# Optimization experiments

Measured on AMD Instinct MI355X. Metric: run time of the kernel, lower is better.

## Reference

```python
import jax, jax.numpy as jnp
import numpy as np

N, T, C, K = 32, 1024, 512, 64
EPS = 1e-12  # torch F.normalize eps


def _l2norm(v, axis):
    n = jnp.sqrt(jnp.sum(v * v, axis=axis, keepdims=True))
    return v / jnp.maximum(n, EPS)


def setup_inputs() -> dict:
    key = jax.random.key(0)
    k1, k2 = jax.random.split(key)
    x = jax.random.normal(k1, (N, T, C), dtype=jnp.float32)
    centroids = jax.random.uniform(k2, (K, C), dtype=jnp.float32)
    # mirrors _init_params: conv.weight = 0.2*centroids, conv.bias = -0.1*||centroids||
    W = 0.2 * centroids
    b = -0.1 * jnp.sqrt(jnp.sum(centroids * centroids, axis=1))
    return {"x": x, "W": W, "b": b, "centroids": centroids}


def reference(x, W, b, centroids):
    # x: [N, T, C] -> [N, C, T]
    xt = jnp.transpose(x, (0, 2, 1))
    # 1x1 Conv1d == per-timestep linear: logits [N, K, T]
    logits = jnp.einsum('kc,nct->nkt', W, xt) + b[None, :, None]
    a = jax.nn.softmax(logits, axis=1)  # softmax over clusters
    # vlad[n,k,c] = sum_t a[n,k,t] * (x[n,c,t] - centroid[k,c])
    #            = (a @ x^T) - sum_t(a) * centroid  (GEMM form, same math)
    vlad = jnp.einsum('nkt,nct->nkc', a, xt) - a.sum(axis=-1)[:, :, None] * centroids[None]
    vlad = _l2norm(vlad, axis=2)          # intra-normalization per cluster
    vlad = vlad.reshape(vlad.shape[0], -1)
    vlad = _l2norm(vlad, axis=1)          # global L2 normalization
    return vlad
```

## Files before the change

kernel.cpp:

```cpp
#include <hip/hip_runtime.h>
#include <cmath>

namespace {

constexpr int N = 32, T = 1024, C = 512, K = 64;
constexpr float EPS = 1e-12f;

typedef short s8v __attribute__((ext_vector_type(8)));
typedef short s4v __attribute__((ext_vector_type(4)));
typedef short s2v __attribute__((ext_vector_type(2)));
typedef float f4v __attribute__((ext_vector_type(4)));

__device__ inline unsigned short f2bh(float f) {
  __bf16 h = (__bf16)f;
  return __builtin_bit_cast(unsigned short, h);
}
__device__ inline float bh2f(unsigned short u) {
  __bf16 h = __builtin_bit_cast(__bf16, u);
  return (float)h;
}

#define MFMA16(A, B, Cc) __builtin_amdgcn_mfma_f32_16x16x32_bf16((A), (B), (Cc), 0, 0, 0)

__global__ __launch_bounds__(256, 4) void k_gemm1(
    const float* __restrict__ x, const float* __restrict__ W,
    const float* __restrict__ b, unsigned short* __restrict__ aTh,
    unsigned short* __restrict__ aTl, float* __restrict__ asum_part) {
  __shared__ __align__(16) unsigned short sm0[4 * 64 * 72];
  __shared__ __align__(16) unsigned short sm1[4 * 64 * 72];
  __shared__ float asum_l[256];

  const int tid = threadIdx.x;
  const int w = tid >> 6, lane = tid & 63, lm = lane & 15, lq = lane >> 4;
  const int th = w >> 1;
  const int kh = w & 1;
  const long r0 = (long)blockIdx.x * 64;
  const int n = blockIdx.x >> 4, tl = blockIdx.x & 15;

  f4v acc[2][2] = {};
  float4 px0[4], pw0[4], px1[4], pw1[4];

#define G1_LOAD(s, c0)                                                       \
  {                                                                          \
    _Pragma("unroll") for (int r = 0; r < 4; ++r) {                          \
      const int f = tid + r * 256, t = f >> 4, cg = f & 15;                  \
      px##s[r] = *(const float4*)&x[(r0 + t) * C + (c0) + cg * 4];           \
      pw##s[r] = *(const float4*)&W[(long)t * C + (c0) + cg * 4];            \
    }                                                                        \
  }

#define G1_STAGE(buf, s)                                                     \
  {                                                                          \
    unsigned short* xh_s = (buf);                                            \
    unsigned short* xl_s = (buf) + 64 * 72;                                  \
    unsigned short* wh_s = (buf) + 2 * 64 * 72;                              \
    unsigned short* wl_s = (buf) + 3 * 64 * 72;                              \
    _Pragma("unroll") for (int r = 0; r < 4; ++r) {                          \
      const int f = tid + r * 256, t = f >> 4, cg = f & 15;                  \
      const float ex[4] = {px##s[r].x, px##s[r].y, px##s[r].z, px##s[r].w};  \
      const float ew[4] = {pw##s[r].x, pw##s[r].y, pw##s[r].z, pw##s[r].w};  \
      s4v xh, xl, wh, wl;                                                    \
      _Pragma("unroll") for (int i = 0; i < 4; ++i) {                        \
        unsigned short hb = f2bh(ex[i]);                                     \
        xh[i] = (short)hb; xl[i] = (short)f2bh(ex[i] - bh2f(hb));            \
        hb = f2bh(ew[i]);                                                    \
        wh[i] = (short)hb; wl[i] = (short)f2bh(ew[i] - bh2f(hb));            \
      }                                                                      \
      *(s4v*)&xh_s[t * 72 + cg * 4] = xh;                                    \
      *(s4v*)&xl_s[t * 72 + cg * 4] = xl;                                    \
      *(s4v*)&wh_s[t * 72 + cg * 4] = wh;                                    \
      *(s4v*)&wl_s[t * 72 + cg * 4] = wl;                                    \
    }                                                                        \
  }

#define G1_MFMA(buf)                                                         \
  {                                                                          \
    unsigned short* xh_s = (buf);                                            \
    unsigned short* xl_s = (buf) + 64 * 72;                                  \
    unsigned short* wh_s = (buf) + 2 * 64 * 72;                              \
    unsigned short* wl_s = (buf) + 3 * 64 * 72;                              \
    _Pragma("unroll") for (int ks = 0; ks < 2; ++ks) {                       \
      const int col = ks * 32 + lq * 8;                                      \
      s8v ah[2], al[2], bh[2], bl[2];                                        \
      _Pragma("unroll") for (int i = 0; i < 2; ++i) {                        \
        ah[i] = *(const s8v*)&xh_s[(th * 32 + i * 16 + lm) * 72 + col];      \
        al[i] = *(const s8v*)&xl_s[(th * 32 + i * 16 + lm) * 72 + col];      \
        bh[i] = *(const s8v*)&wh_s[(kh * 32 + i * 16 + lm) * 72 + col];      \
        bl[i] = *(const s8v*)&wl_s[(kh * 32 + i * 16 + lm) * 72 + col];      \
      }                                                                      \
      _Pragma("unroll") for (int i = 0; i < 2; ++i)                          \
          _Pragma("unroll") for (int j = 0; j < 2; ++j) {                    \
        acc[i][j] = MFMA16(ah[i], bh[j], acc[i][j]);                         \
        acc[i][j] = MFMA16(ah[i], bl[j], acc[i][j]);                         \
        acc[i][j] = MFMA16(al[i], bh[j], acc[i][j]);                         \
      }                                                                      \
    }                                                                        \
  }

  G1_LOAD(0, 0);
  G1_STAGE(sm0, 0);
  G1_LOAD(1, 64);
  __syncthreads();
  for (int c0 = 0; c0 < C; c0 += 128) {
    if (c0 + 128 < C) G1_LOAD(0, c0 + 128);
    G1_STAGE(sm1, 1);
    G1_MFMA(sm0);
    __syncthreads();
    if (c0 + 192 < C) G1_LOAD(1, c0 + 192);
    if (c0 + 128 < C) G1_STAGE(sm0, 0);
    G1_MFMA(sm1);
    __syncthreads();
  }
#undef G1_LOAD
#undef G1_STAGE
#undef G1_MFMA

  float* Ls = (float*)sm0;
  unsigned short* L2h = sm1;
  unsigned short* L2l = sm1 + 64 * 72;
  const float bias[2] = {b[kh * 32 + lm], b[kh * 32 + 16 + lm]};
#pragma unroll
  for (int i = 0; i < 2; ++i)
#pragma unroll
    for (int j = 0; j < 2; ++j)
#pragma unroll
      for (int r = 0; r < 4; ++r)
        Ls[(th * 32 + i * 16 + lq * 4 + r) * 68 + kh * 32 + j * 16 + lm] =
            acc[i][j][r] + bias[j];
  __syncthreads();

  {
    const int row = tid >> 2, q = tid & 3;
    float av[16];
#pragma unroll
    for (int u = 0; u < 4; ++u)
      *(float4*)&av[u * 4] = *(const float4*)&Ls[row * 68 + q * 16 + u * 4];
    float m = av[0];
#pragma unroll
    for (int i = 1; i < 16; ++i) m = fmaxf(m, av[i]);
    m = fmaxf(m, __shfl_xor(m, 1, 64));
    m = fmaxf(m, __shfl_xor(m, 2, 64));
    float sum = 0.f;
#pragma unroll
    for (int i = 0; i < 16; ++i) {
      av[i] = __expf(av[i] - m);
      sum += av[i];
    }
    sum += __shfl_xor(sum, 1, 64);
    sum += __shfl_xor(sum, 2, 64);
    const float inv = 1.f / sum;
    float ps[16];
#pragma unroll
    for (int i = 0; i < 16; ++i) {
      av[i] *= inv;
      ps[i] = av[i];
      const unsigned short hb = f2bh(av[i]);
      L2h[(q * 16 + i) * 72 + row] = hb;
      L2l[(q * 16 + i) * 72 + row] = f2bh(av[i] - bh2f(hb));
    }
#pragma unroll
    for (int s = 4; s < 64; s <<= 1)
#pragma unroll
      for (int i = 0; i < 16; ++i) ps[i] += __shfl_xor(ps[i], s, 64);
    if (lane < 4) {
#pragma unroll
      for (int i = 0; i < 16; ++i) asum_l[w * 64 + q * 16 + i] = ps[i];
    }
  }
  __syncthreads();

  if (tid < 64) {
    asum_part[(n * 16 + tl) * 64 + tid] = asum_l[tid] + asum_l[64 + tid] +
                                          asum_l[128 + tid] + asum_l[192 + tid];
  }
  {
    const int k = tid >> 2, tg = tid & 3;
    const long gb = ((long)n * K + k) * T + tl * 64 + tg * 16;
    *(s8v*)&aTh[gb] = *(const s8v*)&L2h[k * 72 + tg * 16];
    *(s8v*)&aTh[gb + 8] = *(const s8v*)&L2h[k * 72 + tg * 16 + 8];
    *(s8v*)&aTl[gb] = *(const s8v*)&L2l[k * 72 + tg * 16];
    *(s8v*)&aTl[gb + 8] = *(const s8v*)&L2l[k * 72 + tg * 16 + 8];
  }
}

__global__ __launch_bounds__(256, 4) void k_gemm2(
    const float* __restrict__ x, const unsigned short* __restrict__ aTh,
    const unsigned short* __restrict__ aTl,
    const float* __restrict__ asum_part, const float* __restrict__ cent,
    float* __restrict__ vlad, float* __restrict__ ssq_part) {
  __shared__ __align__(16) unsigned short smA[(2 * 64 + 2 * 32) * 72];
  __shared__ __align__(16) unsigned short smB[(2 * 64 + 2 * 32) * 72];
  __shared__ float asum_l[64];
  __shared__ float ssq_l[128];

  const int tid = threadIdx.x;
  const int w = tid >> 6, lane = tid & 63, lm = lane & 15, lq = lane >> 4;
  const int kh = w >> 1;
  const int ch = w & 1;
  const int p = blockIdx.x;
  const int g = p >> 3;
  const int n = ((g & 3) << 3) | (p & 7);
  const int cq = g >> 2;
  const int c0 = cq * 32;

  if (tid < 64) {
    float s = 0.f;
#pragma unroll
    for (int tl = 0; tl < 16; ++tl) s += asum_part[(n * 16 + tl) * 64 + tid];
    asum_l[tid] = s;
  }

  f4v acc[2] = {};
  const int ak = tid >> 2, atg = tid & 3;
  s8v pah0[2], pal0[2], pah1[2], pal1[2];
  float4 px0[2], px1[2];

#define G2_LOAD(s, t0)                                                       \
  {                                                                          \
    const long ab = ((long)n * K + ak) * T + (t0) + atg * 16;                \
    pah##s[0] = *(const s8v*)&aTh[ab];                                       \
    pah##s[1] = *(const s8v*)&aTh[ab + 8];                                   \
    pal##s[0] = *(const s8v*)&aTl[ab];                                       \
    pal##s[1] = *(const s8v*)&aTl[ab + 8];                                   \
    const int cg = tid & 7, tq = tid >> 3;                                   \
    _Pragma("unroll") for (int i = 0; i < 2; ++i)                            \
        px##s[i] = *(const float4*)&x[((long)n * T + (t0) + tq * 2 + i) * C +\
                                      c0 + cg * 4];                          \
  }

#define G2_STAGE(buf, s)                                                     \
  {                                                                          \
    unsigned short* ah_s = (buf);                                            \
    unsigned short* al_s = (buf) + 64 * 72;                                  \
    unsigned short* xh_s = (buf) + 2 * 64 * 72;                              \
    unsigned short* xl_s = (buf) + 2 * 64 * 72 + 32 * 72;                    \
    *(s8v*)&ah_s[ak * 72 + atg * 16] = pah##s[0];                            \
    *(s8v*)&ah_s[ak * 72 + atg * 16 + 8] = pah##s[1];                        \
    *(s8v*)&al_s[ak * 72 + atg * 16] = pal##s[0];                            \
    *(s8v*)&al_s[ak * 72 + atg * 16 + 8] = pal##s[1];                        \
    const int cg = tid & 7, tq = tid >> 3;                                   \
    _Pragma("unroll") for (int cc = 0; cc < 4; ++cc) {                       \
      s2v h, l;                                                              \
      _Pragma("unroll") for (int i = 0; i < 2; ++i) {                        \
        const float e = ((const float*)&px##s[i])[cc];                       \
        const unsigned short hb = f2bh(e);                                   \
        h[i] = (short)hb;                                                    \
        l[i] = (short)f2bh(e - bh2f(hb));                                    \
      }                                                                      \
      *(s2v*)&xh_s[(cg * 4 + cc) * 72 + tq * 2] = h;                         \
      *(s2v*)&xl_s[(cg * 4 + cc) * 72 + tq * 2] = l;                         \
    }                                                                        \
  }

#define G2_MFMA(buf)                                                         \
  {                                                                          \
    unsigned short* ah_s = (buf);                                            \
    unsigned short* al_s = (buf) + 64 * 72;                                  \
    unsigned short* xh_s = (buf) + 2 * 64 * 72;                              \
    unsigned short* xl_s = (buf) + 2 * 64 * 72 + 32 * 72;                    \
    _Pragma("unroll") for (int ks = 0; ks < 2; ++ks) {                       \
      const int col = ks * 32 + lq * 8;                                      \
      s8v ah[2], al[2];                                                      \
      _Pragma("unroll") for (int i = 0; i < 2; ++i) {                        \
        ah[i] = *(const s8v*)&ah_s[(kh * 32 + i * 16 + lm) * 72 + col];      \
        al[i] = *(const s8v*)&al_s[(kh * 32 + i * 16 + lm) * 72 + col];      \
      }                                                                      \
      const s8v bh = *(const s8v*)&xh_s[(ch * 16 + lm) * 72 + col];          \
      const s8v bl = *(const s8v*)&xl_s[(ch * 16 + lm) * 72 + col];          \
      _Pragma("unroll") for (int i = 0; i < 2; ++i) {                        \
        acc[i] = MFMA16(ah[i], bh, acc[i]);                                  \
        acc[i] = MFMA16(ah[i], bl, acc[i]);                                  \
        acc[i] = MFMA16(al[i], bh, acc[i]);                                  \
      }                                                                      \
    }                                                                        \
  }

  G2_LOAD(0, 0);
  G2_STAGE(smA, 0);
  G2_LOAD(1, 64);
  __syncthreads();
  for (int t0 = 0; t0 < T; t0 += 128) {
    if (t0 + 128 < T) G2_LOAD(0, t0 + 128);
    G2_STAGE(smB, 1);
    G2_MFMA(smA);
    __syncthreads();
    if (t0 + 192 < T) G2_LOAD(1, t0 + 192);
    if (t0 + 128 < T) G2_STAGE(smA, 0);
    G2_MFMA(smB);
    __syncthreads();
  }
#undef G2_LOAD
#undef G2_STAGE
#undef G2_MFMA

  float ssqp[2][4];
#pragma unroll
  for (int i = 0; i < 2; ++i) {
#pragma unroll
    for (int r = 0; r < 4; ++r) {
      const int k = kh * 32 + i * 16 + lq * 4 + r;
      const float as = asum_l[k];
      const int c = c0 + ch * 16 + lm;
      const float v = acc[i][r] - as * cent[(long)k * C + c];
      vlad[((long)n * K + k) * C + c] = v;
      ssqp[i][r] = v * v;
    }
  }
#pragma unroll
  for (int i = 0; i < 2; ++i)
#pragma unroll
    for (int r = 0; r < 4; ++r) {
      float s = ssqp[i][r];
      s += __shfl_xor(s, 1, 64);
      s += __shfl_xor(s, 2, 64);
      s += __shfl_xor(s, 4, 64);
      s += __shfl_xor(s, 8, 64);
      ssqp[i][r] = s;
    }
  if (lm == 0) {
#pragma unroll
    for (int i = 0; i < 2; ++i)
#pragma unroll
      for (int r = 0; r < 4; ++r)
        ssq_l[(kh * 32 + i * 16 + lq * 4 + r) * 2 + ch] = ssqp[i][r];
  }
  __syncthreads();
  if (tid < 64)
    ssq_part[(n * 16 + cq) * 64 + tid] = ssq_l[tid * 2] + ssq_l[tid * 2 + 1];
}

__global__ __launch_bounds__(256) void k_norm(
    const float* __restrict__ vlad, const float* __restrict__ ssq_part,
    float* __restrict__ out) {
  __shared__ float denom[64];
  __shared__ float contrib[64];
  __shared__ float ginv;

  const int tid = threadIdx.x;
  const int n = blockIdx.x >> 4;
  const int chunk = blockIdx.x & 15;

  if (tid < 64) {
    float ss = 0.f;
#pragma unroll
    for (int q = 0; q < 16; ++q) ss += ssq_part[(n * 16 + q) * 64 + tid];
    const float d = fmaxf(sqrtf(ss), EPS);
    denom[tid] = d;
    contrib[tid] = ss / (d * d);
  }
  __syncthreads();
  if (tid == 0) {
    float s = 0.f;
#pragma unroll
    for (int k = 0; k < K; ++k) s += contrib[k];
    ginv = 1.0f / fmaxf(sqrtf(s), EPS);
  }
  __syncthreads();

#pragma unroll
  for (int q = 0; q < 2; ++q) {
    const int f4 = tid + q * 256;
    const long off = chunk * 2048 + (long)f4 * 4;
    const int k = (int)(off >> 9);
    float4 v = *(const float4*)&vlad[(long)n * K * C + off];
    const float sc = ginv / denom[k];
    v.x *= sc; v.y *= sc; v.z *= sc; v.w *= sc;
    *(float4*)&out[(long)n * K * C + off] = v;
  }
}

}

extern "C" void kernel_launch(void* const* d_in, const int* in_sizes, int n_in,
                              void* d_out, int out_size, void* d_ws,
                              size_t ws_size, hipStream_t stream) {
  const float* x = reinterpret_cast<const float*>(d_in[0]);
  const float* W = reinterpret_cast<const float*>(d_in[1]);
  const float* b = reinterpret_cast<const float*>(d_in[2]);
  const float* cent = reinterpret_cast<const float*>(d_in[3]);
  float* out = reinterpret_cast<float*>(d_out);

  char* pp = reinterpret_cast<char*>(d_ws);
  unsigned short* aTh = reinterpret_cast<unsigned short*>(pp);
  pp += (size_t)N * K * T * sizeof(unsigned short);
  unsigned short* aTl = reinterpret_cast<unsigned short*>(pp);
  pp += (size_t)N * K * T * sizeof(unsigned short);
  float* vlad = reinterpret_cast<float*>(pp);
  pp += (size_t)N * K * C * sizeof(float);
  float* asum_part = reinterpret_cast<float*>(pp);
  pp += (size_t)512 * 64 * sizeof(float);
  float* ssq_part = reinterpret_cast<float*>(pp);

  k_gemm1<<<(N * T) / 64, 256, 0, stream>>>(x, W, b, aTh, aTl, asum_part);
  k_gemm2<<<N * 16, 256, 0, stream>>>(x, aTh, aTl, asum_part, cent, vlad,
                                      ssq_part);
  k_norm<<<N * 16, 256, 0, stream>>>(vlad, ssq_part, out);
}
```

Measured before the change: 127.3 us.

## Fuse normalization into GEMM2 via last-block atomic ticket per batch

After: 176.6 us. +38.8%, slower.

```diff
diff --git a/kernel.cpp b/kernel.cpp
--- a/kernel.cpp
+++ b/kernel.cpp
@@ -25,7 +25,8 @@
 __global__ __launch_bounds__(256, 4) void k_gemm1(
     const float* __restrict__ x, const float* __restrict__ W,
     const float* __restrict__ b, unsigned short* __restrict__ aTh,
-    unsigned short* __restrict__ aTl, float* __restrict__ asum_part) {
+    unsigned short* __restrict__ aTl, float* __restrict__ asum_part,
+    unsigned int* __restrict__ cnt) {
   __shared__ __align__(16) unsigned short sm0[4 * 64 * 72];
   __shared__ __align__(16) unsigned short sm1[4 * 64 * 72];
   __shared__ float asum_l[256];
@@ -36,6 +37,8 @@
   const int kh = w & 1;
   const long r0 = (long)blockIdx.x * 64;
   const int n = blockIdx.x >> 4, tl = blockIdx.x & 15;
+
+  if (tl == 0 && tid == 0) cnt[n] = 0u;
 
   f4v acc[2][2] = {};
   float4 px0[4], pw0[4], px1[4], pw1[4];
@@ -187,11 +190,14 @@
     const float* __restrict__ x, const unsigned short* __restrict__ aTh,
     const unsigned short* __restrict__ aTl,
     const float* __restrict__ asum_part, const float* __restrict__ cent,
-    float* __restrict__ vlad, float* __restrict__ ssq_part) {
+    float* __restrict__ out, float* __restrict__ ssq_part,
+    unsigned int* __restrict__ cnt) {
   __shared__ __align__(16) unsigned short smA[(2 * 64 + 2 * 32) * 72];
   __shared__ __align__(16) unsigned short smB[(2 * 64 + 2 * 32) * 72];
   __shared__ float asum_l[64];
   __shared__ float ssq_l[128];
+  __shared__ unsigned int ticket;
+  __shared__ float ginv_s;
 
   const int tid = threadIdx.x;
   const int w = tid >> 6, lane = tid & 63, lm = lane & 15, lq = lane >> 4;
@@ -302,7 +308,7 @@
       const float as = asum_l[k];
       const int c = c0 + ch * 16 + lm;
       const float v = acc[i][r] - as * cent[(long)k * C + c];
-      vlad[((long)n * K + k) * C + c] = v;
+      out[((long)n * K + k) * C + c] = v;
       ssqp[i][r] = v * v;
     }
   }
@@ -327,19 +333,16 @@
   __syncthreads();
   if (tid < 64)
     ssq_part[(n * 16 + cq) * 64 + tid] = ssq_l[tid * 2] + ssq_l[tid * 2 + 1];
-}
-
-__global__ __launch_bounds__(256) void k_norm(
-    const float* __restrict__ vlad, const float* __restrict__ ssq_part,
-    float* __restrict__ out) {
-  __shared__ float denom[64];
-  __shared__ float contrib[64];
-  __shared__ float ginv;
-
-  const int tid = threadIdx.x;
-  const int n = blockIdx.x >> 4;
-  const int chunk = blockIdx.x & 15;
-
+
+  __threadfence();
+  __syncthreads();
+  if (tid == 0) ticket = atomicAdd(&cnt[n], 1u);
+  __syncthreads();
+  if (ticket != 15u) return;
+  __threadfence();
+
+  float* denom = (float*)smA;
+  float* contrib = denom + 64;
   if (tid < 64) {
     float ss = 0.f;
 #pragma unroll
@@ -353,16 +356,16 @@
     float s = 0.f;
 #pragma unroll
     for (int k = 0; k < K; ++k) s += contrib[k];
-    ginv = 1.0f / fmaxf(sqrtf(s), EPS);
-  }
-  __syncthreads();
-
-#pragma unroll
-  for (int q = 0; q < 2; ++q) {
-    const int f4 = tid + q * 256;
-    const long off = chunk * 2048 + (long)f4 * 4;
+    ginv_s = 1.0f / fmaxf(sqrtf(s), EPS);
+  }
+  __syncthreads();
+  const float ginv = ginv_s;
+
+#pragma unroll
+  for (int q = 0; q < 32; ++q) {
+    const long off = (long)(tid + q * 256) * 4;
     const int k = (int)(off >> 9);
-    float4 v = *(const float4*)&vlad[(long)n * K * C + off];
+    float4 v = *(const float4*)&out[(long)n * K * C + off];
     const float sc = ginv / denom[k];
     v.x *= sc; v.y *= sc; v.z *= sc; v.w *= sc;
     *(float4*)&out[(long)n * K * C + off] = v;
@@ -385,14 +388,13 @@
   pp += (size_t)N * K * T * sizeof(unsigned short);
   unsigned short* aTl = reinterpret_cast<unsigned short*>(pp);
   pp += (size_t)N * K * T * sizeof(unsigned short);
-  float* vlad = reinterpret_cast<float*>(pp);
-  pp += (size_t)N * K * C * sizeof(float);
   float* asum_part = reinterpret_cast<float*>(pp);
   pp += (size_t)512 * 64 * sizeof(float);
   float* ssq_part = reinterpret_cast<float*>(pp);
-
-  k_gemm1<<<(N * T) / 64, 256, 0, stream>>>(x, W, b, aTh, aTl, asum_part);
-  k_gemm2<<<N * 16, 256, 0, stream>>>(x, aTh, aTl, asum_part, cent, vlad,
-                                      ssq_part);
-  k_norm<<<N * 16, 256, 0, stream>>>(vlad, ssq_part, out);
-}
+  pp += (size_t)512 * 64 * sizeof(float);
+  unsigned int* cnt = reinterpret_cast<unsigned int*>(pp);
+
+  k_gemm1<<<(N * T) / 64, 256, 0, stream>>>(x, W, b, aTh, aTl, asum_part, cnt);
+  k_gemm2<<<N * 16, 256, 0, stream>>>(x, aTh, aTl, asum_part, cent, out,
+                                      ssq_part, cnt);
+}
```

## Widen gemm2 channel tile to 64 with 512-thread blocks

Applied to the files above, without the earlier changes.

Result: slower. 130.7 us (+2.7%).

```diff
diff --git a/kernel.cpp b/kernel.cpp
--- a/kernel.cpp
+++ b/kernel.cpp
@@ -183,25 +183,25 @@
   }
 }
 
-__global__ __launch_bounds__(256, 4) void k_gemm2(
+__global__ __launch_bounds__(512, 2) void k_gemm2(
     const float* __restrict__ x, const unsigned short* __restrict__ aTh,
     const unsigned short* __restrict__ aTl,
     const float* __restrict__ asum_part, const float* __restrict__ cent,
     float* __restrict__ vlad, float* __restrict__ ssq_part) {
-  __shared__ __align__(16) unsigned short smA[(2 * 64 + 2 * 32) * 72];
-  __shared__ __align__(16) unsigned short smB[(2 * 64 + 2 * 32) * 72];
+  __shared__ __align__(16) unsigned short smA[4 * 64 * 72];
+  __shared__ __align__(16) unsigned short smB[4 * 64 * 72];
   __shared__ float asum_l[64];
-  __shared__ float ssq_l[128];
+  __shared__ float ssq_l[256];
 
   const int tid = threadIdx.x;
   const int w = tid >> 6, lane = tid & 63, lm = lane & 15, lq = lane >> 4;
-  const int kh = w >> 1;
-  const int ch = w & 1;
+  const int kh = w >> 2;
+  const int cw = w & 3;
   const int p = blockIdx.x;
   const int g = p >> 3;
   const int n = ((g & 3) << 3) | (p & 7);
   const int cq = g >> 2;
-  const int c0 = cq * 32;
+  const int c0 = cq * 64;
 
   if (tid < 64) {
     float s = 0.f;
@@ -211,18 +211,16 @@
   }
 
   f4v acc[2] = {};
-  const int ak = tid >> 2, atg = tid & 3;
-  s8v pah0[2], pal0[2], pah1[2], pal1[2];
+  const int ak = tid >> 3, atg = tid & 7;
+  s8v pah0, pal0, pah1, pal1;
   float4 px0[2], px1[2];
 
 #define G2_LOAD(s, t0)                                                       \
   {                                                                          \
-    const long ab = ((long)n * K + ak) * T + (t0) + atg * 16;                \
-    pah##s[0] = *(const s8v*)&aTh[ab];                                       \
-    pah##s[1] = *(const s8v*)&aTh[ab + 8];                                   \
-    pal##s[0] = *(const s8v*)&aTl[ab];                                       \
-    pal##s[1] = *(const s8v*)&aTl[ab + 8];                                   \
-    const int cg = tid & 7, tq = tid >> 3;                                   \
+    const long ab = ((long)n * K + ak) * T + (t0) + atg * 8;                 \
+    pah##s = *(const s8v*)&aTh[ab];                                          \
+    pal##s = *(const s8v*)&aTl[ab];                                          \
+    const int cg = tid & 15, tq = tid >> 4;                                  \
     _Pragma("unroll") for (int i = 0; i < 2; ++i)                            \
         px##s[i] = *(const float4*)&x[((long)n * T + (t0) + tq * 2 + i) * C +\
                                       c0 + cg * 4];                          \
@@ -233,12 +231,10 @@
     unsigned short* ah_s = (buf);                                            \
     unsigned short* al_s = (buf) + 64 * 72;                                  \
     unsigned short* xh_s = (buf) + 2 * 64 * 72;                              \
-    unsigned short* xl_s = (buf) + 2 * 64 * 72 + 32 * 72;                    \
-    *(s8v*)&ah_s[ak * 72 + atg * 16] = pah##s[0];                            \
-    *(s8v*)&ah_s[ak * 72 + atg * 16 + 8] = pah##s[1];                        \
-    *(s8v*)&al_s[ak * 72 + atg * 16] = pal##s[0];                            \
-    *(s8v*)&al_s[ak * 72 + atg * 16 + 8] = pal##s[1];                        \
-    const int cg = tid & 7, tq = tid >> 3;                                   \
+    unsigned short* xl_s = (buf) + 3 * 64 * 72;                              \
+    *(s8v*)&ah_s[ak * 72 + atg * 8] = pah##s;                                \
+    *(s8v*)&al_s[ak * 72 + atg * 8] = pal##s;                                \
+    const int cg = tid & 15, tq = tid >> 4;                                  \
     _Pragma("unroll") for (int cc = 0; cc < 4; ++cc) {                       \
       s2v h, l;                                                              \
       _Pragma("unroll") for (int i = 0; i < 2; ++i) {                        \
@@ -257,7 +253,7 @@
     unsigned short* ah_s = (buf);                                            \
     unsigned short* al_s = (buf) + 64 * 72;                                  \
     unsigned short* xh_s = (buf) + 2 * 64 * 72;                              \
-    unsigned short* xl_s = (buf) + 2 * 64 * 72 + 32 * 72;                    \
+    unsigned short* xl_s = (buf) + 3 * 64 * 72;                              \
     _Pragma("unroll") for (int ks = 0; ks < 2; ++ks) {                       \
       const int col = ks * 32 + lq * 8;                                      \
       s8v ah[2], al[2];                                                      \
@@ -265,8 +261,8 @@
         ah[i] = *(const s8v*)&ah_s[(kh * 32 + i * 16 + lm) * 72 + col];      \
         al[i] = *(const s8v*)&al_s[(kh * 32 + i * 16 + lm) * 72 + col];      \
       }                                                                      \
-      const s8v bh = *(const s8v*)&xh_s[(ch * 16 + lm) * 72 + col];          \
-      const s8v bl = *(const s8v*)&xl_s[(ch * 16 + lm) * 72 + col];          \
+      const s8v bh = *(const s8v*)&xh_s[(cw * 16 + lm) * 72 + col];          \
+      const s8v bl = *(const s8v*)&xl_s[(cw * 16 + lm) * 72 + col];          \
       _Pragma("unroll") for (int i = 0; i < 2; ++i) {                        \
         acc[i] = MFMA16(ah[i], bh, acc[i]);                                  \
         acc[i] = MFMA16(ah[i], bl, acc[i]);                                  \
@@ -300,7 +296,7 @@
     for (int r = 0; r < 4; ++r) {
       const int k = kh * 32 + i * 16 + lq * 4 + r;
       const float as = asum_l[k];
-      const int c = c0 + ch * 16 + lm;
+      const int c = c0 + cw * 16 + lm;
       const float v = acc[i][r] - as * cent[(long)k * C + c];
       vlad[((long)n * K + k) * C + c] = v;
       ssqp[i][r] = v * v;
@@ -322,11 +318,12 @@
     for (int i = 0; i < 2; ++i)
 #pragma unroll
       for (int r = 0; r < 4; ++r)
-        ssq_l[(kh * 32 + i * 16 + lq * 4 + r) * 2 + ch] = ssqp[i][r];
+        ssq_l[(kh * 32 + i * 16 + lq * 4 + r) * 4 + cw] = ssqp[i][r];
   }
   __syncthreads();
   if (tid < 64)
-    ssq_part[(n * 16 + cq) * 64 + tid] = ssq_l[tid * 2] + ssq_l[tid * 2 + 1];
+    ssq_part[(n * 8 + cq) * 64 + tid] = ssq_l[tid * 4] + ssq_l[tid * 4 + 1] +
+                                        ssq_l[tid * 4 + 2] + ssq_l[tid * 4 + 3];
 }
 
 __global__ __launch_bounds__(256) void k_norm(
@@ -343,7 +340,7 @@
   if (tid < 64) {
     float ss = 0.f;
 #pragma unroll
-    for (int q = 0; q < 16; ++q) ss += ssq_part[(n * 16 + q) * 64 + tid];
+    for (int q = 0; q < 8; ++q) ss += ssq_part[(n * 8 + q) * 64 + tid];
     const float d = fmaxf(sqrtf(ss), EPS);
     denom[tid] = d;
     contrib[tid] = ss / (d * d);
@@ -392,7 +389,7 @@
   float* ssq_part = reinterpret_cast<float*>(pp);
 
   k_gemm1<<<(N * T) / 64, 256, 0, stream>>>(x, W, b, aTh, aTl, asum_part);
-  k_gemm2<<<N * 16, 256, 0, stream>>>(x, aTh, aTl, asum_part, cent, vlad,
-                                      ssq_part);
+  k_gemm2<<<N * 8, 512, 0, stream>>>(x, aTh, aTl, asum_part, cent, vlad,
+                                     ssq_part);
   k_norm<<<N * 16, 256, 0, stream>>>(vlad, ssq_part, out);
 }
```
